# Kernel tuning notes

Measured on AMD Instinct MI355X. Metric: run time of the kernel, lower is better.

Reference implementation:

```python
import jax, jax.numpy as jnp
import numpy as np

H = 1024  # hidden_size


def _cell(x, W, b):
    # x: [S, B, D_in]; W: [4H, D_in]; b: [4H]
    # One big batched matmul over all timesteps (no recurrence exists).
    gates = jnp.einsum('sbd,gd->sbg', x, W) + b  # [S, B, 4H]
    i, f, g, o = jnp.split(gates, 4, axis=-1)
    i = jax.nn.sigmoid(i)
    g = jnp.tanh(g)
    o = jax.nn.sigmoid(o)
    c = i * g
    h = o * jnp.tanh(c)
    return h, c


def setup_inputs() -> dict:
    key = jax.random.key(0)
    ks = jax.random.split(key, 9)
    S, B, D = 2048, 8, 1024
    s = 1.0 / np.sqrt(D)
    s2 = 1.0 / np.sqrt(2 * H)
    return {
        'x': jax.random.normal(ks[0], (S, B, D), dtype=jnp.float32),
        'W_f0': jax.random.uniform(ks[1], (4 * H, D), jnp.float32, -s, s),
        'b_f0': jax.random.uniform(ks[2], (4 * H,), jnp.float32, -s, s),
        'W_b0': jax.random.uniform(ks[3], (4 * H, D), jnp.float32, -s, s),
        'b_b0': jax.random.uniform(ks[4], (4 * H,), jnp.float32, -s, s),
        'W_f1': jax.random.uniform(ks[5], (4 * H, 2 * H), jnp.float32, -s2, s2),
        'b_f1': jax.random.uniform(ks[6], (4 * H,), jnp.float32, -s2, s2),
        'W_b1': jax.random.uniform(ks[7], (4 * H, 2 * H), jnp.float32, -s2, s2),
        'b_b1': jax.random.uniform(ks[8], (4 * H,), jnp.float32, -s2, s2),
    }


def reference(x, W_f0, b_f0, W_b0, b_b0, W_f1, b_f1, W_b1, b_b1):
    out = x
    h_ns, c_ns = [], []
    for (Wf, bf, Wb, bb) in [(W_f0, b_f0, W_b0, b_b0), (W_f1, b_f1, W_b1, b_b1)]:
        h_f, c_f = _cell(out, Wf, bf)  # forward direction
        h_b, c_b = _cell(out, Wb, bb)  # backward direction (same per-t math)
        out = jnp.concatenate([h_f, h_b], axis=-1)  # [S, B, 2H]
        # forward final state is at t = S-1; backward final state at t = 0
        h_ns += [h_f[-1], h_b[0]]
        c_ns += [c_f[-1], c_b[0]]
    h_n = jnp.stack(h_ns, axis=0)  # [num_layers*2, B, H]
    c_n = jnp.stack(c_ns, axis=0)
    return out, h_n, c_n
```

## Files before the change

### kernel.cpp

```cpp
#include <hip/hip_runtime.h>
#include <hip/hip_bf16.h>

#define S_LEN 2048
#define BATCH 8
#define HID   1024
#define NP    3072
#define MROWS 16384

using bf16x8 = __attribute__((ext_vector_type(8))) short;
using f32x4  = __attribute__((ext_vector_type(4))) float;

__device__ __forceinline__ unsigned short f2b(float f) {
  unsigned int u = __builtin_bit_cast(unsigned int, f);
  u += 0x7fffu + ((u >> 16) & 1u);
  return (unsigned short)(u >> 16);
}

__device__ __forceinline__ void load_lds16(const void* g, void* l) {
  __builtin_amdgcn_global_load_lds(
      (const __attribute__((address_space(1))) void*)g,
      (__attribute__((address_space(3))) void*)(unsigned int)(unsigned long long)l,
      16, 0, 0);
}

#define MEMFENCE asm volatile("" ::: "memory")
#define BARRIER  do { MEMFENCE; __builtin_amdgcn_s_barrier(); MEMFENCE; } while (0)

__global__ void cvt_f32_bf16(const float* __restrict__ in,
                             unsigned short* __restrict__ out, int n4) {
  int i = blockIdx.x * blockDim.x + threadIdx.x;
  if (i >= n4) return;
  const float4 v = reinterpret_cast<const float4*>(in)[i];
  ushort4 u;
  u.x = f2b(v.x); u.y = f2b(v.y); u.z = f2b(v.z); u.w = f2b(v.w);
  reinterpret_cast<ushort4*>(out)[i] = u;
}

__global__ void permute_w(const float* __restrict__ W,
                          unsigned short* __restrict__ Wp, int K) {
  long i = ((long)blockIdx.x * blockDim.x + threadIdx.x) * 4;
  int np = (int)(i / K);
  if (np >= NP) return;
  int k0 = (int)(i % K);
  int chunk = np / 48, rem = np % 48;
  int g3 = rem >> 4, hl = rem & 15;
  int og = (g3 == 0) ? 0 : (g3 == 1) ? 2 : 3;
  int n  = og * 1024 + chunk * 16 + hl;
  const float4 v = *reinterpret_cast<const float4*>(W + (long)n * K + k0);
  ushort4 u;
  u.x = f2b(v.x); u.y = f2b(v.y); u.z = f2b(v.z); u.w = f2b(v.w);
  *reinterpret_cast<ushort4*>(Wp + i) = u;
}

__global__ void permute_b(const float* __restrict__ b, float* __restrict__ bp) {
  int np = blockIdx.x * blockDim.x + threadIdx.x;
  if (np >= NP) return;
  int chunk = np / 48, rem = np % 48;
  int g3 = rem >> 4, hl = rem & 15;
  int og = (g3 == 0) ? 0 : (g3 == 1) ? 2 : 3;
  bp[np] = b[og * 1024 + chunk * 16 + hl];
}

template <int MODE>
__global__ void __launch_bounds__(256, 2)
lstm_gemm(const unsigned short* __restrict__ A,
          const unsigned short* __restrict__ WpF,
          const unsigned short* __restrict__ WpB,
          const float* __restrict__ bpF, const float* __restrict__ bpB,
          int K,
          unsigned short* __restrict__ out_bf, float* __restrict__ out_f,
          float* __restrict__ hn, float* __restrict__ cn) {
  __shared__ __align__(16) char lds[81920];

  const int dir = blockIdx.z;
  const unsigned short* __restrict__ Wp = dir ? WpB : WpF;
  const float* __restrict__ bp = dir ? bpB : bpF;
  const int bm = blockIdx.y;
  const int bn = blockIdx.x;

  const int tid  = threadIdx.x;
  const int wid  = tid >> 6;
  const int lane = tid & 63;
  const int wm   = wid >> 1;
  const int wn   = wid & 1;

  const int  nt = K >> 6;
  const long K2 = (long)K * 2;

  const int rlane = lane >> 3;
  const int cb    = (((lane & 7) ^ rlane) << 4);
  const char* Asrc = (const char*)A  + ((long)bm * 128 + rlane) * K2 + cb;
  const char* Bsrc = (const char*)Wp + ((long)bn * 192 + rlane) * K2 + cb;

  const int l15 = lane & 15;
  const int hi  = lane >> 4;
  const int c0  = ((hi ^ (l15 & 7)) << 4);
  const int aro = (wm * 64 + l15) * 128;
  const int bro = 16384 + (wn * 96 + l15) * 128;

  f32x4 acc[4][6];
  const f32x4 zero = {0.f, 0.f, 0.f, 0.f};
#pragma unroll
  for (int i = 0; i < 4; ++i)
#pragma unroll
    for (int j = 0; j < 6; ++j) acc[i][j] = zero;

  auto STAGE = [&](int t) {
    if (t >= nt) return;
    char* d = lds + (t & 1) * 40960;
    const long off = (long)t * 128;
#pragma unroll
    for (int s = 0; s < 4; ++s) {
      const int slot = s * 4 + wid;
      load_lds16(Asrc + (long)(slot * 8) * K2 + off, d + slot * 1024);
    }
#pragma unroll
    for (int s = 0; s < 6; ++s) {
      const int slot = s * 4 + wid;
      load_lds16(Bsrc + (long)(slot * 8) * K2 + off, d + 16384 + slot * 1024);
    }
  };

  STAGE(0);
  asm volatile("s_waitcnt vmcnt(0)" ::: "memory");
  BARRIER;

  for (int t = 0; t < nt; ++t) {
    STAGE(t + 1);

    const char* buf = lds + (t & 1) * 40960;
    bf16x8 a[4][2], b[6][2];
#pragma unroll
    for (int nf = 0; nf < 6; ++nf) {
      b[nf][0] = *(const bf16x8*)(buf + bro + nf * 2048 + c0);
      b[nf][1] = *(const bf16x8*)(buf + bro + nf * 2048 + (c0 ^ 64));
    }
#pragma unroll
    for (int mf = 0; mf < 4; ++mf) {
      a[mf][0] = *(const bf16x8*)(buf + aro + mf * 2048 + c0);
      a[mf][1] = *(const bf16x8*)(buf + aro + mf * 2048 + (c0 ^ 64));
    }

    __builtin_amdgcn_s_setprio(1);
#pragma unroll
    for (int mf = 0; mf < 4; ++mf)
#pragma unroll
      for (int nf = 0; nf < 6; ++nf) {
        acc[mf][nf] = __builtin_amdgcn_mfma_f32_16x16x32_bf16(
            a[mf][0], b[nf][0], acc[mf][nf], 0, 0, 0);
        acc[mf][nf] = __builtin_amdgcn_mfma_f32_16x16x32_bf16(
            a[mf][1], b[nf][1], acc[mf][nf], 0, 0, 0);
      }
    __builtin_amdgcn_s_setprio(0);

    asm volatile("s_waitcnt vmcnt(0)" ::: "memory");
    BARRIER;
  }

  const int col    = l15;
  const int rbase  = hi * 4;
  const int chunk0 = bn * 4 + wn * 2;
  const int Lidx   = MODE * 2 + dir;

#pragma unroll
  for (int hg = 0; hg < 2; ++hg) {
    const int chunk  = chunk0 + hg;
    const int h      = chunk * 16 + col;
    const int outcol = dir * HID + h;
    const float bi = bp[chunk * 48 + col];
    const float bg = bp[chunk * 48 + 16 + col];
    const float bo = bp[chunk * 48 + 32 + col];
#pragma unroll
    for (int mf = 0; mf < 4; ++mf) {
#pragma unroll
      for (int r = 0; r < 4; ++r) {
        const int m = bm * 128 + wm * 64 + mf * 16 + rbase + r;
        const float iv = acc[mf][hg * 3 + 0][r] + bi;
        const float gv = acc[mf][hg * 3 + 1][r] + bg;
        const float ov = acc[mf][hg * 3 + 2][r] + bo;
        const float is = 1.f / (1.f + __expf(-iv));
        const float gt = tanhf(gv);
        const float os = 1.f / (1.f + __expf(-ov));
        const float c  = is * gt;
        const float hv = os * tanhf(c);
        if (MODE == 0) {
          out_bf[(long)m * 2048 + outcol] = f2b(hv);
        } else {
          out_f[(long)m * 2048 + outcol] = hv;
        }
        const bool wst = (dir == 0) ? (m >= (S_LEN - 1) * BATCH) : (m < BATCH);
        if (wst) {
          const int b = (dir == 0) ? (m - (S_LEN - 1) * BATCH) : m;
          hn[((long)Lidx * BATCH + b) * HID + h] = hv;
          cn[((long)Lidx * BATCH + b) * HID + h] = c;
        }
      }
    }
  }
}

extern "C" void kernel_launch(void* const* d_in, const int* in_sizes, int n_in,
                              void* d_out, int out_size, void* d_ws, size_t ws_size,
                              hipStream_t stream) {
  const float* x    = (const float*)d_in[0];
  const float* W_f0 = (const float*)d_in[1];
  const float* b_f0 = (const float*)d_in[2];
  const float* W_b0 = (const float*)d_in[3];
  const float* b_b0 = (const float*)d_in[4];
  const float* W_f1 = (const float*)d_in[5];
  const float* b_f1 = (const float*)d_in[6];
  const float* W_b1 = (const float*)d_in[7];
  const float* b_b1 = (const float*)d_in[8];

  float* out = (float*)d_out;
  float* hn  = out + (long)MROWS * 2048;
  float* cn  = hn + 4 * BATCH * HID;

  unsigned short* x_bf  = (unsigned short*)d_ws;
  unsigned short* out1  = x_bf + (long)MROWS * 1024;
  unsigned short* wp_f0 = out1 + (long)MROWS * 2048;
  unsigned short* wp_b0 = wp_f0 + (long)NP * 1024;
  unsigned short* wp_f1 = wp_b0 + (long)NP * 1024;
  unsigned short* wp_b1 = wp_f1 + (long)NP * 2048;
  float* bp_f0 = (float*)(wp_b1 + (long)NP * 2048);
  float* bp_b0 = bp_f0 + NP;
  float* bp_f1 = bp_b0 + NP;
  float* bp_b1 = bp_f1 + NP;

  cvt_f32_bf16<<<16384, 256, 0, stream>>>(x, x_bf, MROWS * 1024 / 4);
  permute_w<<<3072, 256, 0, stream>>>(W_f0, wp_f0, 1024);
  permute_w<<<3072, 256, 0, stream>>>(W_b0, wp_b0, 1024);
  permute_w<<<6144, 256, 0, stream>>>(W_f1, wp_f1, 2048);
  permute_w<<<6144, 256, 0, stream>>>(W_b1, wp_b1, 2048);
  permute_b<<<12, 256, 0, stream>>>(b_f0, bp_f0);
  permute_b<<<12, 256, 0, stream>>>(b_b0, bp_b0);
  permute_b<<<12, 256, 0, stream>>>(b_f1, bp_f1);
  permute_b<<<12, 256, 0, stream>>>(b_b1, bp_b1);

  dim3 grid(NP / 192, MROWS / 128, 2);
  lstm_gemm<0><<<grid, 256, 0, stream>>>(x_bf, wp_f0, wp_b0, bp_f0, bp_b0, 1024,
                                         out1, nullptr, hn, cn);
  lstm_gemm<1><<<grid, 256, 0, stream>>>(out1, wp_f1, wp_b1, bp_f1, bp_b1, 2048,
                                         nullptr, out, hn, cn);
}
```

Measured before the change: 657.0 us.

## Fuse prep kernels, remap GEMM block order, use exp-based tanh

Merges the nine conversion and permutation launches into one prep kernel that picks its job from the block index, which removes per-launch overhead. The GEMM grid gets a block-index remap so concurrently running blocks are spread across XCD-strided groups, meant to improve L2 reuse of A and W tiles. tanhf is replaced with an __expf-based formula to shorten the epilogue. The exp form may lose some accuracy or overflow to inf for large inputs, and the remap assumes the grid is exactly 16x128.

```diff
diff --git a/kernel.cpp b/kernel.cpp
--- a/kernel.cpp
+++ b/kernel.cpp
@@ -16,6 +16,13 @@
   return (unsigned short)(u >> 16);
 }
 
+__device__ __forceinline__ float sigf(float x) {
+  return 1.f / (1.f + __expf(-x));
+}
+__device__ __forceinline__ float tanh_f(float x) {
+  return 2.f / (1.f + __expf(-2.f * x)) - 1.f;
+}
+
 __device__ __forceinline__ void load_lds16(const void* g, void* l) {
   __builtin_amdgcn_global_load_lds(
       (const __attribute__((address_space(1))) void*)g,
@@ -26,39 +33,58 @@
 #define MEMFENCE asm volatile("" ::: "memory")
 #define BARRIER  do { MEMFENCE; __builtin_amdgcn_s_barrier(); MEMFENCE; } while (0)
 
-__global__ void cvt_f32_bf16(const float* __restrict__ in,
-                             unsigned short* __restrict__ out, int n4) {
-  int i = blockIdx.x * blockDim.x + threadIdx.x;
-  if (i >= n4) return;
-  const float4 v = reinterpret_cast<const float4*>(in)[i];
-  ushort4 u;
-  u.x = f2b(v.x); u.y = f2b(v.y); u.z = f2b(v.z); u.w = f2b(v.w);
-  reinterpret_cast<ushort4*>(out)[i] = u;
-}
-
-__global__ void permute_w(const float* __restrict__ W,
-                          unsigned short* __restrict__ Wp, int K) {
-  long i = ((long)blockIdx.x * blockDim.x + threadIdx.x) * 4;
-  int np = (int)(i / K);
-  if (np >= NP) return;
-  int k0 = (int)(i % K);
-  int chunk = np / 48, rem = np % 48;
-  int g3 = rem >> 4, hl = rem & 15;
-  int og = (g3 == 0) ? 0 : (g3 == 1) ? 2 : 3;
-  int n  = og * 1024 + chunk * 16 + hl;
+__device__ __forceinline__ void permute_w_dev(const float* __restrict__ W,
+                                              unsigned short* __restrict__ Wp,
+                                              long id, int K) {
+  const long i = id * 4;
+  const int np = (int)(i / K);
+  const int k0 = (int)(i % K);
+  const int chunk = np / 48, rem = np % 48;
+  const int g3 = rem >> 4, hl = rem & 15;
+  const int og = (g3 == 0) ? 0 : (g3 == 1) ? 2 : 3;
+  const int n  = og * 1024 + chunk * 16 + hl;
   const float4 v = *reinterpret_cast<const float4*>(W + (long)n * K + k0);
   ushort4 u;
   u.x = f2b(v.x); u.y = f2b(v.y); u.z = f2b(v.z); u.w = f2b(v.w);
   *reinterpret_cast<ushort4*>(Wp + i) = u;
 }
 
-__global__ void permute_b(const float* __restrict__ b, float* __restrict__ bp) {
-  int np = blockIdx.x * blockDim.x + threadIdx.x;
-  if (np >= NP) return;
-  int chunk = np / 48, rem = np % 48;
-  int g3 = rem >> 4, hl = rem & 15;
-  int og = (g3 == 0) ? 0 : (g3 == 1) ? 2 : 3;
-  bp[np] = b[og * 1024 + chunk * 16 + hl];
+__global__ void prep(const float* __restrict__ x, unsigned short* __restrict__ x_bf,
+                     const float* __restrict__ Wf0, const float* __restrict__ Wb0,
+                     const float* __restrict__ Wf1, const float* __restrict__ Wb1,
+                     unsigned short* __restrict__ pf0, unsigned short* __restrict__ pb0,
+                     unsigned short* __restrict__ pf1, unsigned short* __restrict__ pb1,
+                     const float* __restrict__ bf0, const float* __restrict__ bb0,
+                     const float* __restrict__ bf1, const float* __restrict__ bb1,
+                     float* __restrict__ bpf0, float* __restrict__ bpb0,
+                     float* __restrict__ bpf1, float* __restrict__ bpb1) {
+  const int blk = blockIdx.x;
+  const int tid = threadIdx.x;
+  if (blk < 16384) {
+    const int i = blk * 256 + tid;
+    const float4 v = reinterpret_cast<const float4*>(x)[i];
+    ushort4 u;
+    u.x = f2b(v.x); u.y = f2b(v.y); u.z = f2b(v.z); u.w = f2b(v.w);
+    reinterpret_cast<ushort4*>(x_bf)[i] = u;
+  } else if (blk < 19456) {
+    permute_w_dev(Wf0, pf0, (long)(blk - 16384) * 256 + tid, 1024);
+  } else if (blk < 22528) {
+    permute_w_dev(Wb0, pb0, (long)(blk - 19456) * 256 + tid, 1024);
+  } else if (blk < 28672) {
+    permute_w_dev(Wf1, pf1, (long)(blk - 22528) * 256 + tid, 2048);
+  } else if (blk < 34816) {
+    permute_w_dev(Wb1, pb1, (long)(blk - 28672) * 256 + tid, 2048);
+  } else {
+    const int r = blk - 34816;
+    const int which = r / 12;
+    const int np = (r % 12) * 256 + tid;
+    const float* bs = which == 0 ? bf0 : which == 1 ? bb0 : which == 2 ? bf1 : bb1;
+    float* bd       = which == 0 ? bpf0 : which == 1 ? bpb0 : which == 2 ? bpf1 : bpb1;
+    const int chunk = np / 48, rem = np % 48;
+    const int g3 = rem >> 4, hl = rem & 15;
+    const int og = (g3 == 0) ? 0 : (g3 == 1) ? 2 : 3;
+    bd[np] = bs[og * 1024 + chunk * 16 + hl];
+  }
 }
 
 template <int MODE>
@@ -75,8 +101,11 @@
   const int dir = blockIdx.z;
   const unsigned short* __restrict__ Wp = dir ? WpB : WpF;
   const float* __restrict__ bp = dir ? bpB : bpF;
-  const int bm = blockIdx.y;
-  const int bn = blockIdx.x;
+
+  const int f    = blockIdx.x + (blockIdx.y << 4);
+  const int virt = (f >> 3) + (f & 7) * 256;
+  const int bm   = virt >> 4;
+  const int bn   = virt & 15;
 
   const int tid  = threadIdx.x;
   const int wid  = tid >> 6;
@@ -178,11 +207,11 @@
         const float iv = acc[mf][hg * 3 + 0][r] + bi;
         const float gv = acc[mf][hg * 3 + 1][r] + bg;
         const float ov = acc[mf][hg * 3 + 2][r] + bo;
-        const float is = 1.f / (1.f + __expf(-iv));
-        const float gt = tanhf(gv);
-        const float os = 1.f / (1.f + __expf(-ov));
+        const float is = sigf(iv);
+        const float gt = tanh_f(gv);
+        const float os = sigf(ov);
         const float c  = is * gt;
-        const float hv = os * tanhf(c);
+        const float hv = os * tanh_f(c);
         if (MODE == 0) {
           out_bf[(long)m * 2048 + outcol] = f2b(hv);
         } else {
@@ -227,17 +256,12 @@
   float* bp_f1 = bp_b0 + NP;
   float* bp_b1 = bp_f1 + NP;
 
-  cvt_f32_bf16<<<16384, 256, 0, stream>>>(x, x_bf, MROWS * 1024 / 4);
-  permute_w<<<3072, 256, 0, stream>>>(W_f0, wp_f0, 1024);
-  permute_w<<<3072, 256, 0, stream>>>(W_b0, wp_b0, 1024);
-  permute_w<<<6144, 256, 0, stream>>>(W_f1, wp_f1, 2048);
-  permute_w<<<6144, 256, 0, stream>>>(W_b1, wp_b1, 2048);
-  permute_b<<<12, 256, 0, stream>>>(b_f0, bp_f0);
-  permute_b<<<12, 256, 0, stream>>>(b_b0, bp_b0);
-  permute_b<<<12, 256, 0, stream>>>(b_f1, bp_f1);
-  permute_b<<<12, 256, 0, stream>>>(b_b1, bp_b1);
-
-  dim3 grid(NP / 192, MROWS / 128, 2);
+  prep<<<34864, 256, 0, stream>>>(x, x_bf, W_f0, W_b0, W_f1, W_b1,
+                                  wp_f0, wp_b0, wp_f1, wp_b1,
+                                  b_f0, b_b0, b_f1, b_b1,
+                                  bp_f0, bp_b0, bp_f1, bp_b1);
+
+  dim3 grid(16, 128, 2);
   lstm_gemm<0><<<grid, 256, 0, stream>>>(x_bf, wp_f0, wp_b0, bp_f0, bp_b0, 1024,
                                          out1, nullptr, hn, cn);
   lstm_gemm<1><<<grid, 256, 0, stream>>>(out1, wp_f1, wp_b1, bp_f1, bp_b1, 2048,
```

Result: no change. 650.2 us (-1.0%).
